# Optimization experiments

Measured on AMD Instinct MI355X. Metric: run time of the kernel, lower is better.

Reference implementation:

```python
import jax, jax.numpy as jnp
import numpy as np

N = 4            # polynomial nodes per segment
SEGMENTS = 32
IN_F = 1024
OUT_F = 1024
BATCH = 32
LENGTH = 2.0
HALF = 0.5 * LENGTH
K = (N - 1) * SEGMENTS + 1  # 97 coefficients per (out,in) pair


def setup_inputs() -> dict:
    key = jax.random.key(0)
    k1, k2 = jax.random.split(key)
    x = jax.random.uniform(k1, (BATCH, IN_F), jnp.float32, -1.0, 1.0)
    wm = 1.0 / IN_F  # uniform_(-weight_magnitude/in_features, +...)
    w = jax.random.uniform(k2, (OUT_F, IN_F, K), jnp.float32, -wm, wm)
    return {"x": x, "w": w}


def _lagrange_basis(x):
    # Chebyshev-Lobatto nodes on [-1, 1]: X_k = -cos(k*pi/(n-1))
    X = -jnp.cos(jnp.arange(N) * (np.pi / (N - 1))).astype(x.dtype)
    eye = jnp.eye(N, dtype=bool)
    D = jnp.where(eye, 1.0, X[:, None] - X[None, :])      # X[j] - X[m], diag -> 1
    diff = x[..., None, None] - X                          # [..., 1, n(m)]
    ratio = jnp.where(eye, 1.0, diff / D)                  # [..., n(j), n(m)]
    return jnp.prod(ratio, axis=-1)                        # [..., n] basis_j(x)


def reference(x, w):
    # segment index per element, clamped to [0, segments-1]
    id_min = jnp.clip(((x + HALF) / LENGTH * SEGMENTS).astype(jnp.int32), 0, SEGMENTS - 1)
    id_max = id_min + 1
    wid_min = id_min * (N - 1)                             # [B, I]
    idx = wid_min[..., None] + jnp.arange(N, dtype=jnp.int32)  # [B, I, n]
    # gather per-element coefficient windows: wsel[b,i,o,j] = w[o,i,idx[b,i,j]]
    w2 = jnp.transpose(w, (1, 0, 2))                       # [I, O, K]
    wsel = jnp.take_along_axis(w2[None], idx[:, :, None, :], axis=3)  # [B, I, O, n]
    # map x into local segment coordinates on [-half, half]
    x_min = 2.0 * id_min.astype(x.dtype) / SEGMENTS - 1.0
    x_max = 2.0 * id_max.astype(x.dtype) / SEGMENTS - 1.0
    x_in = LENGTH * (x - x_min) / (x_max - x_min) - HALF   # [B, I]
    basis = _lagrange_basis(x_in)                          # [B, I, n]
    # sum over in_features and nodes: 'ijk,jkli->jl' in the original repo
    return jnp.einsum('bin,bion->bo', basis, wsel)
```

## Files before the change

kernel.cpp:

```cpp
#include <hip/hip_runtime.h>

#define IN_F   1024
#define OUT_F  1024
#define KCOEF  97
#define RPW    256
#define RPC    8
#define NCH    (RPW / RPC)
#define CFL    (RPC * KCOEF)

typedef float f4 __attribute__((ext_vector_type(4)));

__global__ __launch_bounds__(256)
void transpose_x(const float* __restrict__ x, float* __restrict__ xT) {
    int t = blockIdx.x * 256 + threadIdx.x;
    int b = t >> 10, i = t & 1023;
    xT[(i << 5) + b] = x[t];
}

#define ISSUE(c) do {                                                     \
    const float* _src = wslice + (c) * CFL;                               \
    _Pragma("unroll")                                                     \
    for (int _u = 0; _u < 12; ++_u) sw[_u] = _src[lane + (_u << 6)];      \
    if (lane < 8) swt = _src[768 + lane];                                 \
    sx = *(const f4*)&xslice[(c) * (RPC * 32) + (lane << 2)];             \
} while (0)

#define WRITE(cb_) do {                                                   \
    float* _dw = shw[wv][cb_];                                            \
    _Pragma("unroll")                                                     \
    for (int _u = 0; _u < 12; ++_u) _dw[lane + (_u << 6)] = sw[_u];       \
    if (lane < 8) _dw[768 + lane] = swt;                                  \
    *(f4*)&shx[wv][cb_][lane << 2] = sx;                                  \
} while (0)

#define COMPUTE(cb_) do {                                                 \
    const float* _rows = shw[wv][cb_];                                    \
    const float* _xr   = shx[wv][cb_];                                    \
    _Pragma("unroll")                                                     \
    for (int _r4 = 0; _r4 < 4; ++_r4) {                                   \
        const int _r = (h << 2) + _r4;                                    \
        float _xv = _xr[(_r << 5) + bb];                                  \
        float _s = (_xv + 1.0f) * 16.0f;                                  \
        int _id = (int)_s;                                                \
        _id = _id < 0 ? 0 : (_id > 31 ? 31 : _id);                        \
        float _d  = _xv - ((float)_id * 0.0625f - 1.0f);                  \
        float _tt = fmaf(_d, 32.0f, -1.0f);                               \
        float _ap = _tt + 1.0f, _bp = _tt + 0.5f;                         \
        float _cm = _tt - 0.5f, _dm = _tt - 1.0f;                         \
        float _uu = _bp * _cm, _vv = _ap * _dm;                           \
        float _B0 = _uu * _dm * (-2.0f / 3.0f);                           \
        float _B1 = _vv * _cm * ( 4.0f / 3.0f);                           \
        float _B2 = _vv * _bp * (-4.0f / 3.0f);                           \
        float _B3 = _uu * _ap * ( 2.0f / 3.0f);                           \
        const float* _row = _rows + _r * KCOEF;                           \
        int _j3 = _id * 3;                                                \
        float _w0 = _row[_j3], _w1 = _row[_j3 + 1];                       \
        float _w2 = _row[_j3 + 2], _w3 = _row[_j3 + 3];                   \
        float _v = fmaf(_B0, _w0, fmaf(_B1, _w1,                          \
                   fmaf(_B2, _w2, _B3 * _w3)));                           \
        if (_r4 & 1) acc1 += _v; else acc0 += _v;                         \
    }                                                                     \
} while (0)

__global__ __launch_bounds__(256, 4)
void piecewise_main(const float* __restrict__ xT,
                    const float* __restrict__ w,
                    float* __restrict__ out) {
    const int bid = blockIdx.x;
    const int o = (bid & 7) * 128 + (bid >> 3);
    const int t    = threadIdx.x;
    const int wv   = t >> 6;
    const int lane = t & 63;
    const int h    = lane >> 5;
    const int bb   = lane & 31;

    __shared__ __align__(16) float shw[4][2][CFL];
    __shared__ __align__(16) float shx[4][2][RPC * 32];
    __shared__ float red[256];

    const float* wslice = w + (size_t)o * (IN_F * KCOEF) + wv * (RPW * KCOEF);
    const float* xslice = xT + wv * (RPW * 32);

    float sw[12], swt;
    f4 sx;
    float acc0 = 0.f, acc1 = 0.f;

    ISSUE(0);
    WRITE(0);

    for (int c = 0; c < NCH; ++c) {
        const int cb = c & 1;
        if (c + 1 < NCH) ISSUE(c + 1);
        COMPUTE(cb);
        if (c + 1 < NCH) WRITE(cb ^ 1);
    }

    red[t] = acc0 + acc1;
    __syncthreads();
    if (t < 32) {
        float sum = red[t];
        #pragma unroll
        for (int gg = 1; gg < 8; ++gg) sum += red[gg * 32 + t];
        out[t * OUT_F + o] = sum;
    }
}

extern "C" void kernel_launch(void* const* d_in, const int* in_sizes, int n_in,
                              void* d_out, int out_size, void* d_ws, size_t ws_size,
                              hipStream_t stream) {
    const float* x = (const float*)d_in[0];
    const float* w = (const float*)d_in[1];
    float*       out = (float*)d_out;
    float*       xT  = (float*)d_ws;

    transpose_x<<<(32 * IN_F) / 256, 256, 0, stream>>>(x, xT);
    piecewise_main<<<OUT_F, 256, 0, stream>>>(xT, w, out);
}
```

Before: 81.77 us.

## Stream weights directly to LDS with triple-buffered async loads and block barriers

After: 80.72 us. Within noise of the previous version (-1.3%).

```diff
diff --git a/kernel.cpp b/kernel.cpp
--- a/kernel.cpp
+++ b/kernel.cpp
@@ -3,67 +3,90 @@
 #define IN_F   1024
 #define OUT_F  1024
 #define KCOEF  97
-#define RPW    256
-#define RPC    8
-#define NCH    (RPW / RPC)
-#define CFL    (RPC * KCOEF)
+#define CROWS  32
+#define CFL    (CROWS * KCOEF)
+#define CB     (CFL * 4)
+#define NCH    32
 
 typedef float f4 __attribute__((ext_vector_type(4)));
 
+#define AS1 __attribute__((address_space(1)))
+#define AS3 __attribute__((address_space(3)))
+
 __global__ __launch_bounds__(256)
-void transpose_x(const float* __restrict__ x, float* __restrict__ xT) {
+void pack_x(const float* __restrict__ x, float* __restrict__ xq) {
     int t = blockIdx.x * 256 + threadIdx.x;
     int b = t >> 10, i = t & 1023;
-    xT[(i << 5) + b] = x[t];
+    xq[((i >> 2) << 7) + (b << 2) + (i & 3)] = x[t];
 }
 
-#define ISSUE(c) do {                                                     \
-    const float* _src = wslice + (c) * CFL;                               \
-    _Pragma("unroll")                                                     \
-    for (int _u = 0; _u < 12; ++_u) sw[_u] = _src[lane + (_u << 6)];      \
-    if (lane < 8) swt = _src[768 + lane];                                 \
-    sx = *(const f4*)&xslice[(c) * (RPC * 32) + (lane << 2)];             \
+#define ISSUE_W(c, buf_) do {                                                   \
+    const char* _gw = wbase + (size_t)(c) * CB;                                 \
+    char* _lw = (char*)&shw[buf_][0];                                           \
+    _Pragma("unroll")                                                           \
+    for (int _k = 0; _k < 3; ++_k)                                              \
+        __builtin_amdgcn_global_load_lds(                                       \
+            (const AS1 void*)(_gw + (_k << 12) + (t << 4)),                     \
+            (AS3 void*)(_lw + (_k << 12) + (wv << 10)), 16, 0, 0);              \
+    if (lane < 2)                                                               \
+        __builtin_amdgcn_global_load_lds(                                       \
+            (const AS1 void*)(_gw + 12288 + (wv << 5) + (lane << 4)),           \
+            (AS3 void*)(_lw + 12288 + (wv << 5)), 16, 0, 0);                    \
 } while (0)
 
-#define WRITE(cb_) do {                                                   \
-    float* _dw = shw[wv][cb_];                                            \
+#define XLOAD(c) (*(const f4*)&xq[((((c) << 3) + g) << 7) + (b << 2)])
+
+#define BASIS(b_, j_, xv_) do {                                           \
     _Pragma("unroll")                                                     \
-    for (int _u = 0; _u < 12; ++_u) _dw[lane + (_u << 6)] = sw[_u];       \
-    if (lane < 8) _dw[768 + lane] = swt;                                  \
-    *(f4*)&shx[wv][cb_][lane << 2] = sx;                                  \
-} while (0)
-
-#define COMPUTE(cb_) do {                                                 \
-    const float* _rows = shw[wv][cb_];                                    \
-    const float* _xr   = shx[wv][cb_];                                    \
-    _Pragma("unroll")                                                     \
-    for (int _r4 = 0; _r4 < 4; ++_r4) {                                   \
-        const int _r = (h << 2) + _r4;                                    \
-        float _xv = _xr[(_r << 5) + bb];                                  \
-        float _s = (_xv + 1.0f) * 16.0f;                                  \
+    for (int _r = 0; _r < 4; ++_r) {                                      \
+        float _x = xv_[_r];                                               \
+        float _s = (_x + 1.0f) * 16.0f;                                   \
         int _id = (int)_s;                                                \
         _id = _id < 0 ? 0 : (_id > 31 ? 31 : _id);                        \
-        float _d  = _xv - ((float)_id * 0.0625f - 1.0f);                  \
+        float _d  = _x - ((float)_id * 0.0625f - 1.0f);                   \
         float _tt = fmaf(_d, 32.0f, -1.0f);                               \
         float _ap = _tt + 1.0f, _bp = _tt + 0.5f;                         \
         float _cm = _tt - 0.5f, _dm = _tt - 1.0f;                         \
         float _uu = _bp * _cm, _vv = _ap * _dm;                           \
-        float _B0 = _uu * _dm * (-2.0f / 3.0f);                           \
-        float _B1 = _vv * _cm * ( 4.0f / 3.0f);                           \
-        float _B2 = _vv * _bp * (-4.0f / 3.0f);                           \
-        float _B3 = _uu * _ap * ( 2.0f / 3.0f);                           \
-        const float* _row = _rows + _r * KCOEF;                           \
-        int _j3 = _id * 3;                                                \
-        float _w0 = _row[_j3], _w1 = _row[_j3 + 1];                       \
-        float _w2 = _row[_j3 + 2], _w3 = _row[_j3 + 3];                   \
-        float _v = fmaf(_B0, _w0, fmaf(_B1, _w1,                          \
-                   fmaf(_B2, _w2, _B3 * _w3)));                           \
-        if (_r4 & 1) acc1 += _v; else acc0 += _v;                         \
+        b_[_r][0] = _uu * _dm * (-2.0f / 3.0f);                           \
+        b_[_r][1] = _vv * _cm * ( 4.0f / 3.0f);                           \
+        b_[_r][2] = _vv * _bp * (-4.0f / 3.0f);                           \
+        b_[_r][3] = _uu * _ap * ( 2.0f / 3.0f);                           \
+        j_[_r] = _id * 3;                                                 \
     }                                                                     \
 } while (0)
 
+#define COMPUTE(b_, j_, buf_) do {                                        \
+    const float* _rows = &shw[buf_][(g << 2) * KCOEF];                    \
+    _Pragma("unroll")                                                     \
+    for (int _r = 0; _r < 4; ++_r) {                                      \
+        const float* _row = _rows + _r * KCOEF;                           \
+        int _j = j_[_r];                                                  \
+        float _w0 = _row[_j], _w1 = _row[_j + 1];                         \
+        float _w2 = _row[_j + 2], _w3 = _row[_j + 3];                     \
+        float _v = fmaf(b_[_r][0], _w0, fmaf(b_[_r][1], _w1,              \
+                   fmaf(b_[_r][2], _w2, b_[_r][3] * _w3)));               \
+        if (_r & 1) acc1 += _v; else acc0 += _v;                          \
+    }                                                                     \
+} while (0)
+
+#define SBAR0() __builtin_amdgcn_sched_barrier(0)
+
+#define WAITBAR(N) do {                                                   \
+    asm volatile("s_waitcnt vmcnt(" #N ")" ::: "memory");                 \
+    SBAR0();                                                              \
+    __builtin_amdgcn_s_barrier();                                         \
+    SBAR0();                                                              \
+} while (0)
+
+#define ENDBAR() do {                                                     \
+    SBAR0();                                                              \
+    __builtin_amdgcn_s_barrier();                                         \
+    SBAR0();                                                              \
+} while (0)
+
 __global__ __launch_bounds__(256, 4)
-void piecewise_main(const float* __restrict__ xT,
+void piecewise_main(const float* __restrict__ xq,
                     const float* __restrict__ w,
                     float* __restrict__ out) {
     const int bid = blockIdx.x;
@@ -71,29 +94,50 @@
     const int t    = threadIdx.x;
     const int wv   = t >> 6;
     const int lane = t & 63;
-    const int h    = lane >> 5;
-    const int bb   = lane & 31;
+    const int g    = t >> 5;
+    const int b    = t & 31;
 
-    __shared__ __align__(16) float shw[4][2][CFL];
-    __shared__ __align__(16) float shx[4][2][RPC * 32];
+    __shared__ __align__(16) float shw[3][CFL];
     __shared__ float red[256];
 
-    const float* wslice = w + (size_t)o * (IN_F * KCOEF) + wv * (RPW * KCOEF);
-    const float* xslice = xT + wv * (RPW * 32);
+    const char* wbase = (const char*)(w + (size_t)o * (IN_F * KCOEF));
 
-    float sw[12], swt;
-    f4 sx;
+    float bA[4][4], bB[4][4];
+    int   jA[4],   jB[4];
     float acc0 = 0.f, acc1 = 0.f;
 
-    ISSUE(0);
-    WRITE(0);
+    f4 xv0 = XLOAD(0);
+    SBAR0();
+    ISSUE_W(0, 0);
+    ISSUE_W(1, 1);
+    BASIS(bA, jA, xv0);
 
-    for (int c = 0; c < NCH; ++c) {
-        const int cb = c & 1;
-        if (c + 1 < NCH) ISSUE(c + 1);
-        COMPUTE(cb);
-        if (c + 1 < NCH) WRITE(cb ^ 1);
+    for (int cc = 0; cc < 30; cc += 2) {
+        const int p0 = cc % 3, p1 = (cc + 1) % 3, p2 = (cc + 2) % 3;
+        f4 xv1 = XLOAD(cc + 1);
+        SBAR0();
+        ISSUE_W(cc + 2, p2);
+        WAITBAR(4);
+        BASIS(bB, jB, xv1);
+        COMPUTE(bA, jA, p0);
+        ENDBAR();
+        f4 xv2 = XLOAD(cc + 2);
+        SBAR0();
+        ISSUE_W(cc + 3, p0);
+        WAITBAR(4);
+        BASIS(bA, jA, xv2);
+        COMPUTE(bB, jB, p1);
+        ENDBAR();
     }
+
+    f4 xv31 = XLOAD(31);
+    asm volatile("s_waitcnt vmcnt(0)" ::: "memory");
+    SBAR0();
+    __builtin_amdgcn_s_barrier();
+    SBAR0();
+    BASIS(bB, jB, xv31);
+    COMPUTE(bA, jA, 0);
+    COMPUTE(bB, jB, 1);
 
     red[t] = acc0 + acc1;
     __syncthreads();
@@ -111,8 +155,8 @@
     const float* x = (const float*)d_in[0];
     const float* w = (const float*)d_in[1];
     float*       out = (float*)d_out;
-    float*       xT  = (float*)d_ws;
+    float*       xq  = (float*)d_ws;
 
-    transpose_x<<<(32 * IN_F) / 256, 256, 0, stream>>>(x, xT);
-    piecewise_main<<<OUT_F, 256, 0, stream>>>(xT, w, out);
+    pack_x<<<(32 * IN_F) / 256, 256, 0, stream>>>(x, xq);
+    piecewise_main<<<OUT_F, 256, 0, stream>>>(xq, w, out);
 }
```
